# Kernel optimization log

Hardware: AMD Instinct MI355X
Metric: run time of the kernel (lower is better)

## Reference

```python
import jax, jax.numpy as jnp
import numpy as np

NEG_SLOPE = 0.2  # PyG GATConv default negative_slope


def gat_conv(x, src, dst, W, a_src, a_dst, bias, concat=True):
    """PyG-style GATConv (self-loops already appended to src/dst).
    x: [N, Fin], W: [Fin, H*C], a_src/a_dst: [H, C], bias: [H*C] or [C].
    """
    N = x.shape[0]
    H, C = a_src.shape
    h = (x @ W).reshape(N, H, C)                       # [N, H, C]
    s_src = jnp.einsum('nhc,hc->nh', h, a_src)         # per-node src logit
    s_dst = jnp.einsum('nhc,hc->nh', h, a_dst)         # per-node dst logit
    e = jax.nn.leaky_relu(s_src[src] + s_dst[dst], NEG_SLOPE)   # [E, H]
    # segment softmax over incoming edges of each destination node
    m = jax.ops.segment_max(e, dst, num_segments=N)    # [N, H]
    ex = jnp.exp(e - m[dst])
    denom = jax.ops.segment_sum(ex, dst, num_segments=N)
    alpha = ex / (denom[dst] + 1e-16)                  # [E, H]
    out = jax.ops.segment_sum(h[src] * alpha[:, :, None], dst, num_segments=N)  # [N,H,C]
    out = out.reshape(N, H * C) if concat else out.mean(axis=1)
    return out + bias


def setup_inputs() -> dict:
    key = jax.random.key(0)
    ks = jax.random.split(key, 12)
    N, E = 20000, 320000
    Fin, Hd, Hh = 384, 256, 4
    x = jax.random.normal(ks[0], (N, Fin), dtype=jnp.float32)
    edge_index = jax.random.randint(ks[1], (2, E), 0, N, dtype=jnp.int32)
    s = lambda k, shp, fan: jax.random.normal(k, shp, dtype=jnp.float32) / np.sqrt(fan)
    return {
        'x': x, 'edge_index': edge_index,
        'W1': s(ks[2], (Fin, Hh * Hd), Fin),
        'a_src1': s(ks[3], (Hh, Hd), Hd), 'a_dst1': s(ks[4], (Hh, Hd), Hd),
        'b1': jnp.zeros((Hh * Hd,), jnp.float32),
        'W2': s(ks[5], (Hh * Hd, Hd), Hh * Hd),
        'a_src2': s(ks[6], (1, Hd), Hd), 'a_dst2': s(ks[7], (1, Hd), Hd),
        'b2': jnp.zeros((Hd,), jnp.float32),
        'Wp1': s(ks[8], (Hd, Hd // 2), Hd), 'bp1': jnp.zeros((Hd // 2,), jnp.float32),
        'Wp2': s(ks[9], (Hd // 2, 1), Hd // 2), 'bp2': jnp.zeros((1,), jnp.float32),
    }


def reference(x, edge_index, W1, a_src1, a_dst1, b1, W2, a_src2, a_dst2, b2,
              Wp1, bp1, Wp2, bp2):
    N = x.shape[0]
    loops = jnp.arange(N, dtype=edge_index.dtype)
    src = jnp.concatenate([edge_index[0], loops])  # PyG add_self_loops=True
    dst = jnp.concatenate([edge_index[1], loops])
    h = jax.nn.elu(gat_conv(x, src, dst, W1, a_src1, a_dst1, b1, concat=True))
    h = jax.nn.elu(gat_conv(h, src, dst, W2, a_src2, a_dst2, b2, concat=True))
    graph_features = jnp.mean(h, axis=0, keepdims=True)  # batch=None path
    infl = jax.nn.sigmoid(jax.nn.relu(h @ Wp1 + bp1) @ Wp2 + bp2)
    return h, graph_features, infl
```

## Files before the change

kernel.cpp:

```cpp
#include <hip/hip_runtime.h>

#define NEG_SLOPE 0.2f

typedef __bf16 bf16x8 __attribute__((ext_vector_type(8)));
typedef float floatx4 __attribute__((ext_vector_type(4)));
typedef unsigned short ushortx4 __attribute__((ext_vector_type(4)));
typedef unsigned short ushortx8 __attribute__((ext_vector_type(8)));

__device__ __forceinline__ float eluf(float x) { return x > 0.f ? x : __expf(x) - 1.f; }
__device__ __forceinline__ float lrelu(float x) { return x > 0.f ? x : NEG_SLOPE * x; }

__device__ __forceinline__ unsigned short f2bf(float f) {
    unsigned u = __float_as_uint(f);
    u += 0x7FFFu + ((u >> 16) & 1u);
    return (unsigned short)(u >> 16);
}
__device__ __forceinline__ float bf2f(unsigned short h) {
    return __uint_as_float(((unsigned)h) << 16);
}

__device__ __forceinline__ void async16(const unsigned short* g, unsigned short* l) {
    __builtin_amdgcn_global_load_lds(
        (const __attribute__((address_space(1))) unsigned int*)g,
        (__attribute__((address_space(3))) unsigned int*)l,
        16, 0, 0);
}

__global__ __launch_bounds__(256) void prep_kernel(
        const int* __restrict__ ei, int E, int N, int* __restrict__ counts,
        const float* __restrict__ x, unsigned short* __restrict__ xb,
        const float* __restrict__ W1, unsigned short* __restrict__ w1t,
        const float* __restrict__ W2, unsigned short* __restrict__ w2t,
        const float* __restrict__ Wp1, unsigned short* __restrict__ wp1t,
        const float* __restrict__ as1, const float* __restrict__ ad1, float* __restrict__ U) {
    __shared__ float tile[32][33];
    int b = blockIdx.x;
    int t = threadIdx.x;
    int Et = E + N;
    int nA = (Et + 255) >> 8;
    int nB = (N * 96 + 255) >> 8;
    if (b < nA) {
        int i = b * 256 + t;
        if (i < Et) {
            int d = (i < E) ? ei[E + i] : (i - E);
            atomicAdd(&counts[d], 1);
        }
    } else if (b < nA + nB) {
        int i = (b - nA) * 256 + t;
        if (i < N * 96) {
            float4 v = ((const float4*)x)[i];
            ushortx4 o;
            o[0] = f2bf(v.x); o[1] = f2bf(v.y); o[2] = f2bf(v.z); o[3] = f2bf(v.w);
            *(ushortx4*)(xb + (size_t)i * 4) = o;
        }
    } else if (b < nA + nB + 384) {
        int idx = b - nA - nB;
        int n0 = (idx & 31) * 32, k0 = (idx >> 5) * 32;
        int tx = t & 31, ty = t >> 5;
        #pragma unroll
        for (int i = 0; i < 32; i += 8)
            tile[ty + i][tx] = W1[(size_t)(k0 + ty + i) * 1024 + n0 + tx];
        __syncthreads();
        #pragma unroll
        for (int i = 0; i < 32; i += 8)
            w1t[(size_t)(n0 + ty + i) * 384 + k0 + tx] = f2bf(tile[tx][ty + i]);
    } else if (b < nA + nB + 384 + 256) {
        int idx = b - nA - nB - 384;
        int n0 = (idx & 7) * 32, k0 = (idx >> 3) * 32;
        int tx = t & 31, ty = t >> 5;
        #pragma unroll
        for (int i = 0; i < 32; i += 8)
            tile[ty + i][tx] = W2[(size_t)(k0 + ty + i) * 256 + n0 + tx];
        __syncthreads();
        #pragma unroll
        for (int i = 0; i < 32; i += 8)
            w2t[(size_t)(n0 + ty + i) * 1024 + k0 + tx] = f2bf(tile[tx][ty + i]);
    } else if (b < nA + nB + 384 + 256 + 32) {
        int idx = b - nA - nB - 384 - 256;
        int n0 = (idx & 3) * 32, k0 = (idx >> 2) * 32;
        int tx = t & 31, ty = t >> 5;
        #pragma unroll
        for (int i = 0; i < 32; i += 8)
            tile[ty + i][tx] = Wp1[(size_t)(k0 + ty + i) * 128 + n0 + tx];
        __syncthreads();
        #pragma unroll
        for (int i = 0; i < 32; i += 8)
            wp1t[(size_t)(n0 + ty + i) * 256 + k0 + tx] = f2bf(tile[tx][ty + i]);
    } else {
        int idx = b - nA - nB - 384 - 256 - 32;
        int k = idx * 4 + (t >> 6);
        int lane = t & 63;
        #pragma unroll
        for (int r = 0; r < 8; r++) {
            int h = r & 3;
            const float* a = (r < 4 ? as1 : ad1) + h * 256 + lane * 4;
            const float* w = W1 + (size_t)k * 1024 + h * 256 + lane * 4;
            float4 wv = *(const float4*)w;
            float4 av = *(const float4*)a;
            float p = wv.x * av.x + wv.y * av.y + wv.z * av.z + wv.w * av.w;
            #pragma unroll
            for (int off = 32; off; off >>= 1) p += __shfl_xor(p, off);
            if (lane == 0) U[r * 384 + k] = p;
        }
    }
}

__global__ void scan_kernel(int* __restrict__ counts_cursor, int* __restrict__ row_ptr, int N) {
    __shared__ int s_wsum[16];
    __shared__ int s_carry;
    int t = threadIdx.x;
    int lane = t & 63, wid = t >> 6;
    if (t == 0) { s_carry = 0; row_ptr[0] = 0; }
    __syncthreads();
    for (int start = 0; start < N; start += 1024) {
        int i = start + t;
        int v = (i < N) ? counts_cursor[i] : 0;
        int s = v;
        #pragma unroll
        for (int d = 1; d < 64; d <<= 1) {
            int u = __shfl_up(s, d);
            if (lane >= d) s += u;
        }
        if (lane == 63) s_wsum[wid] = s;
        __syncthreads();
        if (wid == 0) {
            int w = (lane < 16) ? s_wsum[lane] : 0;
            #pragma unroll
            for (int d = 1; d < 16; d <<= 1) {
                int u = __shfl_up(w, d);
                if (lane >= d) w += u;
            }
            if (lane < 16) s_wsum[lane] = w;
        }
        __syncthreads();
        int incl = s + (wid ? s_wsum[wid - 1] : 0) + s_carry;
        if (i < N) { row_ptr[i + 1] = incl; counts_cursor[i] = incl - v; }
        __syncthreads();
        if (t == 0) s_carry += s_wsum[15];
        __syncthreads();
    }
}

__global__ void fill_kernel(const int* __restrict__ ei, int E, int N,
                            int* __restrict__ cursor, int* __restrict__ col) {
    int i = blockIdx.x * blockDim.x + threadIdx.x;
    int Et = E + N;
    if (i >= Et) return;
    int s, d;
    if (i < E) { s = ei[i]; d = ei[E + i]; } else { s = d = i - E; }
    int pos = atomicAdd(&cursor[d], 1);
    col[pos] = s;
}

__global__ void sU_kernel(const unsigned short* __restrict__ xb, const float* __restrict__ U,
                          float* __restrict__ ss1, float* __restrict__ sd1, int N) {
    int wid = (blockIdx.x * blockDim.x + threadIdx.x) >> 6;
    int lane = threadIdx.x & 63;
    if (wid >= N) return;
    int half = lane >> 5, l32 = lane & 31;
    int c0 = l32 * 12;
    const unsigned short* row = xb + (size_t)wid * 384 + c0;
    ushortx8 v8 = *(const ushortx8*)row;
    ushortx4 v4 = *(const ushortx4*)(row + 8);
    float xv[12];
    #pragma unroll
    for (int j = 0; j < 8; j++) xv[j] = bf2f(v8[j]);
    #pragma unroll
    for (int j = 0; j < 4; j++) xv[8 + j] = bf2f(v4[j]);
    float p[4];
    #pragma unroll
    for (int r = 0; r < 4; r++) {
        const float* u = U + (half * 4 + r) * 384 + c0;
        float s = 0.f;
        #pragma unroll
        for (int j = 0; j < 12; j++) s += xv[j] * u[j];
        #pragma unroll
        for (int off = 16; off; off >>= 1) s += __shfl_xor(s, off);
        p[r] = s;
    }
    if (l32 == 0) {
        float* dst = half ? (sd1 + wid * 4) : (ss1 + wid * 4);
        dst[0] = p[0]; dst[1] = p[1]; dst[2] = p[2]; dst[3] = p[3];
    }
}

__global__ void s2_kernel(const unsigned short* __restrict__ h2b, const float* __restrict__ a_src,
                          const float* __restrict__ a_dst, float* __restrict__ ssrc,
                          float* __restrict__ sdst, int N) {
    int wid = (blockIdx.x * blockDim.x + threadIdx.x) >> 6;
    int lane = threadIdx.x & 63;
    if (wid >= N) return;
    ushortx4 v = *(const ushortx4*)(h2b + (size_t)wid * 256 + lane * 4);
    float4 a = ((const float4*)a_src)[lane];
    float4 d = ((const float4*)a_dst)[lane];
    float v0 = bf2f(v[0]), v1 = bf2f(v[1]), v2 = bf2f(v[2]), v3 = bf2f(v[3]);
    float s = v0 * a.x + v1 * a.y + v2 * a.z + v3 * a.w;
    float t = v0 * d.x + v1 * d.y + v2 * d.z + v3 * d.w;
    for (int off = 32; off; off >>= 1) { s += __shfl_xor(s, off); t += __shfl_xor(t, off); }
    if (lane == 0) { ssrc[wid] = s; sdst[wid] = t; }
}

__global__ __launch_bounds__(256) void alpha1_kernel(const float* __restrict__ ssrc,
        const float* __restrict__ sdst, const int* __restrict__ row_ptr,
        const int* __restrict__ col, float* __restrict__ wx, float* __restrict__ den, int N) {
    int wid = (blockIdx.x * blockDim.x + threadIdx.x) >> 6;
    int lane = threadIdx.x & 63;
    if (wid >= N) return;
    int base = row_ptr[wid];
    int deg = row_ptr[wid + 1] - base;
    float sd0 = sdst[wid * 4 + 0], sd1 = sdst[wid * 4 + 1];
    float sd2 = sdst[wid * 4 + 2], sd3 = sdst[wid * 4 + 3];
    float m0 = -1e30f, m1 = -1e30f, m2 = -1e30f, m3 = -1e30f;
    for (int i = lane; i < deg; i += 64) {
        int s = col[base + i];
        const float* sp = ssrc + s * 4;
        m0 = fmaxf(m0, lrelu(sp[0] + sd0));
        m1 = fmaxf(m1, lrelu(sp[1] + sd1));
        m2 = fmaxf(m2, lrelu(sp[2] + sd2));
        m3 = fmaxf(m3, lrelu(sp[3] + sd3));
    }
    #pragma unroll
    for (int off = 32; off; off >>= 1) {
        m0 = fmaxf(m0, __shfl_xor(m0, off));
        m1 = fmaxf(m1, __shfl_xor(m1, off));
        m2 = fmaxf(m2, __shfl_xor(m2, off));
        m3 = fmaxf(m3, __shfl_xor(m3, off));
    }
    float d0 = 0.f, d1 = 0.f, d2 = 0.f, d3 = 0.f;
    for (int i = lane; i < deg; i += 64) {
        int s = col[base + i];
        const float* sp = ssrc + s * 4;
        float4 w4;
        w4.x = __expf(lrelu(sp[0] + sd0) - m0); d0 += w4.x;
        w4.y = __expf(lrelu(sp[1] + sd1) - m1); d1 += w4.y;
        w4.z = __expf(lrelu(sp[2] + sd2) - m2); d2 += w4.z;
        w4.w = __expf(lrelu(sp[3] + sd3) - m3); d3 += w4.w;
        *(float4*)(wx + (size_t)(base + i) * 4) = w4;
    }
    #pragma unroll
    for (int off = 32; off; off >>= 1) {
        d0 += __shfl_xor(d0, off);
        d1 += __shfl_xor(d1, off);
        d2 += __shfl_xor(d2, off);
        d3 += __shfl_xor(d3, off);
    }
    if (lane == 0) {
        den[wid * 4 + 0] = d0; den[wid * 4 + 1] = d1;
        den[wid * 4 + 2] = d2; den[wid * 4 + 3] = d3;
    }
}

__global__ __launch_bounds__(256) void alpha2_kernel(const float* __restrict__ ssrc,
        const float* __restrict__ sdst, const int* __restrict__ row_ptr,
        const int* __restrict__ col, float* __restrict__ wx, float* __restrict__ den, int N) {
    int wid = (blockIdx.x * blockDim.x + threadIdx.x) >> 6;
    int lane = threadIdx.x & 63;
    if (wid >= N) return;
    int base = row_ptr[wid];
    int deg = row_ptr[wid + 1] - base;
    float sd = sdst[wid];
    float m = -1e30f;
    for (int i = lane; i < deg; i += 64) {
        int s = col[base + i];
        m = fmaxf(m, lrelu(ssrc[s] + sd));
    }
    #pragma unroll
    for (int off = 32; off; off >>= 1) m = fmaxf(m, __shfl_xor(m, off));
    float d = 0.f;
    for (int i = lane; i < deg; i += 64) {
        int s = col[base + i];
        float x = __expf(lrelu(ssrc[s] + sd) - m);
        d += x;
        wx[base + i] = x;
    }
    #pragma unroll
    for (int off = 32; off; off >>= 1) d += __shfl_xor(d, off);
    if (lane == 0) den[wid] = d;
}

__global__ __launch_bounds__(256) void aggx_kernel(const unsigned short* __restrict__ xb,
        const float* __restrict__ wx, const float* __restrict__ den,
        const int* __restrict__ row_ptr, const int* __restrict__ col,
        unsigned short* __restrict__ aggxn, int N) {
    __shared__ unsigned short lds[4][1536];
    int t = threadIdx.x;
    int wv = t >> 6;
    int wid = blockIdx.x * 4 + wv;
    int lane = t & 63;
    bool active = wid < N;
    int half = lane >> 5, l32 = lane & 31;
    int c0 = l32 * 12;
    if (active) {
        int base = row_ptr[wid];
        int deg = row_ptr[wid + 1] - base;
        float acc[4][12] = {};
        for (int i = half; i < deg; i += 2) {
            int e = base + i;
            int s = col[e];
            float4 w4 = *(const float4*)(wx + (size_t)e * 4);
            const unsigned short* row = xb + (size_t)s * 384 + c0;
            ushortx8 v8 = *(const ushortx8*)row;
            ushortx4 v4 = *(const ushortx4*)(row + 8);
            float xv[12];
            #pragma unroll
            for (int j = 0; j < 8; j++) xv[j] = bf2f(v8[j]);
            #pragma unroll
            for (int j = 0; j < 4; j++) xv[8 + j] = bf2f(v4[j]);
            #pragma unroll
            for (int j = 0; j < 12; j++) {
                acc[0][j] += w4.x * xv[j];
                acc[1][j] += w4.y * xv[j];
                acc[2][j] += w4.z * xv[j];
                acc[3][j] += w4.w * xv[j];
            }
        }
        #pragma unroll
        for (int h = 0; h < 4; h++)
            #pragma unroll
            for (int j = 0; j < 12; j++)
                acc[h][j] += __shfl_xor(acc[h][j], 32);
        #pragma unroll
        for (int hh = 0; hh < 2; hh++) {
            int h = half * 2 + hh;
            float inv = 1.f / (den[wid * 4 + h] + 1e-16f);
            ushortx8 o8; ushortx4 o4;
            #pragma unroll
            for (int j = 0; j < 8; j++) {
                float v = half ? acc[2 + hh][j] : acc[hh][j];
                o8[j] = f2bf(v * inv);
            }
            #pragma unroll
            for (int j = 0; j < 4; j++) {
                float v = half ? acc[2 + hh][8 + j] : acc[hh][8 + j];
                o4[j] = f2bf(v * inv);
            }
            unsigned short* lp = &lds[wv][h * 384 + c0];
            *(ushortx8*)lp = o8;
            *(ushortx4*)(lp + 8) = o4;
        }
    }
    __syncthreads();
    size_t blockBase = (size_t)blockIdx.x * 4 * 1536;
    const unsigned short* lflat = &lds[0][0];
    #pragma unroll
    for (int j = 0; j < 3; j++) {
        int so = j * 2048 + t * 8;
        int node = blockIdx.x * 4 + so / 1536;
        if (node < N)
            *(ushortx8*)(aggxn + blockBase + so) = *(const ushortx8*)(lflat + so);
    }
}

#define LDK 40

__global__ __launch_bounds__(256) void gemm_l1(const unsigned short* __restrict__ A,
        const unsigned short* __restrict__ Bt, const float* __restrict__ bias,
        unsigned short* __restrict__ Cout, int M) {
    __shared__ unsigned short As[2][128 * 32];
    __shared__ unsigned short Bs[2][128 * 32];
    int t = threadIdx.x;
    int lane = t & 63, wave = t >> 6;
    int wm = (wave >> 1) * 64, wn = (wave & 1) * 64;
    int q = lane >> 4, l16 = lane & 15;
    int row0 = blockIdx.y * 128, col0 = blockIdx.x * 128;
    int hoff = (col0 >> 8) * 384;
    floatx4 acc[4][4] = {};
    int srow = t >> 2, skc = (t & 3) * 8;
    const unsigned short* Ag0 = A + (size_t)min(row0 + srow, M - 1) * 1536 + hoff + skc;
    const unsigned short* Ag1 = A + (size_t)min(row0 + srow + 64, M - 1) * 1536 + hoff + skc;
    const unsigned short* Bg0 = Bt + (size_t)(col0 + srow) * 384 + skc;
    const unsigned short* Bg1 = Bt + (size_t)(col0 + srow + 64) * 384 + skc;
#define STG_L1(buf, kt) \
    async16(Ag0 + (kt), &As[buf][t * 8]); \
    async16(Ag1 + (kt), &As[buf][2048 + t * 8]); \
    async16(Bg0 + (kt), &Bs[buf][t * 8]); \
    async16(Bg1 + (kt), &Bs[buf][2048 + t * 8]);
    STG_L1(0, 0)
    __syncthreads();
    #pragma unroll
    for (int ti = 0; ti < 12; ++ti) {
        int cur = ti & 1;
        if (ti < 11) { STG_L1(cur ^ 1, (ti + 1) * 32) }
        __builtin_amdgcn_sched_barrier(0);
        bf16x8 af[4], bfr[4];
        #pragma unroll
        for (int i = 0; i < 4; i++)
            af[i] = *(const bf16x8*)&As[cur][(wm + i * 16 + l16) * 32 + q * 8];
        #pragma unroll
        for (int j = 0; j < 4; j++)
            bfr[j] = *(const bf16x8*)&Bs[cur][(wn + j * 16 + l16) * 32 + q * 8];
        #pragma unroll
        for (int i = 0; i < 4; i++)
            #pragma unroll
            for (int j = 0; j < 4; j++)
                acc[i][j] = __builtin_amdgcn_mfma_f32_16x16x32_bf16(af[i], bfr[j], acc[i][j], 0, 0, 0);
        __syncthreads();
    }
#undef STG_L1
    float bj[4];
    #pragma unroll
    for (int j = 0; j < 4; j++) bj[j] = bias[col0 + wn + l16 + j * 16];
    #pragma unroll
    for (int i = 0; i < 4; i++) {
        #pragma unroll
        for (int r = 0; r < 4; r++) {
            int grow = row0 + wm + i * 16 + q * 4 + r;
            if (grow < M) {
                unsigned short* cp = Cout + (size_t)grow * 1024 + col0 + wn + l16;
                #pragma unroll
                for (int j = 0; j < 4; j++) cp[j * 16] = f2bf(eluf(acc[i][j][r] + bj[j]));
            }
        }
    }
}

__global__ __launch_bounds__(256) void gemm_l2(const unsigned short* __restrict__ A,
        const unsigned short* __restrict__ Bt, unsigned short* __restrict__ Cout, int M) {
    __shared__ unsigned short As[2][128 * 32];
    __shared__ unsigned short Bs[2][64 * 32];
    int t = threadIdx.x;
    int lane = t & 63, wave = t >> 6;
    int wm = (wave >> 1) * 64, wn = (wave & 1) * 32;
    int q = lane >> 4, l16 = lane & 15;
    int row0 = blockIdx.y * 128, col0 = blockIdx.x * 64;
    floatx4 acc[4][2] = {};
    int srow = t >> 2, skc = (t & 3) * 8;
    const unsigned short* Ag0 = A + (size_t)min(row0 + srow, M - 1) * 1024 + skc;
    const unsigned short* Ag1 = A + (size_t)min(row0 + srow + 64, M - 1) * 1024 + skc;
    const unsigned short* Bg0 = Bt + (size_t)(col0 + srow) * 1024 + skc;
#define STG_L2(buf, kt) \
    async16(Ag0 + (kt), &As[buf][t * 8]); \
    async16(Ag1 + (kt), &As[buf][2048 + t * 8]); \
    async16(Bg0 + (kt), &Bs[buf][t * 8]);
    STG_L2(0, 0)
    __syncthreads();
    #pragma unroll
    for (int ti = 0; ti < 32; ++ti) {
        int cur = ti & 1;
        if (ti < 31) { STG_L2(cur ^ 1, (ti + 1) * 32) }
        __builtin_amdgcn_sched_barrier(0);
        bf16x8 af[4], bfr[2];
        #pragma unroll
        for (int i = 0; i < 4; i++)
            af[i] = *(const bf16x8*)&As[cur][(wm + i * 16 + l16) * 32 + q * 8];
        #pragma unroll
        for (int j = 0; j < 2; j++)
            bfr[j] = *(const bf16x8*)&Bs[cur][(wn + j * 16 + l16) * 32 + q * 8];
        #pragma unroll
        for (int i = 0; i < 4; i++)
            #pragma unroll
            for (int j = 0; j < 2; j++)
                acc[i][j] = __builtin_amdgcn_mfma_f32_16x16x32_bf16(af[i], bfr[j], acc[i][j], 0, 0, 0);
        __syncthreads();
    }
#undef STG_L2
    #pragma unroll
    for (int i = 0; i < 4; i++) {
        #pragma unroll
        for (int r = 0; r < 4; r++) {
            int grow = row0 + wm + i * 16 + q * 4 + r;
            if (grow < M) {
                unsigned short* cp = Cout + (size_t)grow * 256 + col0 + wn + l16;
                #pragma unroll
                for (int j = 0; j < 2; j++) cp[j * 16] = f2bf(acc[i][j][r]);
            }
        }
    }
}

__global__ __launch_bounds__(256) void agg2_kernel(const unsigned short* __restrict__ h2b,
        const float* __restrict__ wx, const float* __restrict__ den,
        const int* __restrict__ row_ptr, const int* __restrict__ col,
        const float* __restrict__ bias, float* __restrict__ out,
        unsigned short* __restrict__ outb, int N) {
    int wid = (blockIdx.x * blockDim.x + threadIdx.x) >> 6;
    int lane = threadIdx.x & 63;
    if (wid >= N) return;
    int base = row_ptr[wid];
    int deg = row_ptr[wid + 1] - base;
    float4 a = {0, 0, 0, 0};
    int c = lane * 4;
    int i = 0;
    for (; i + 1 < deg; i += 2) {
        int s0 = col[base + i], s1 = col[base + i + 1];
        float x0 = wx[base + i], x1 = wx[base + i + 1];
        ushortx4 v0 = *(const ushortx4*)(h2b + (size_t)s0 * 256 + c);
        ushortx4 v1 = *(const ushortx4*)(h2b + (size_t)s1 * 256 + c);
        a.x += x0 * bf2f(v0[0]) + x1 * bf2f(v1[0]);
        a.y += x0 * bf2f(v0[1]) + x1 * bf2f(v1[1]);
        a.z += x0 * bf2f(v0[2]) + x1 * bf2f(v1[2]);
        a.w += x0 * bf2f(v0[3]) + x1 * bf2f(v1[3]);
    }
    if (i < deg) {
        int s0 = col[base + i];
        float x0 = wx[base + i];
        ushortx4 v0 = *(const ushortx4*)(h2b + (size_t)s0 * 256 + c);
        a.x += x0 * bf2f(v0[0]); a.y += x0 * bf2f(v0[1]);
        a.z += x0 * bf2f(v0[2]); a.w += x0 * bf2f(v0[3]);
    }
    float inv = 1.f / (den[wid] + 1e-16f);
    float4 o;
    o.x = eluf(a.x * inv + bias[c + 0]);
    o.y = eluf(a.y * inv + bias[c + 1]);
    o.z = eluf(a.z * inv + bias[c + 2]);
    o.w = eluf(a.w * inv + bias[c + 3]);
    *(float4*)(out + (size_t)wid * 256 + c) = o;
    ushortx4 ob;
    ob[0] = f2bf(o.x); ob[1] = f2bf(o.y); ob[2] = f2bf(o.z); ob[3] = f2bf(o.w);
    *(ushortx4*)(outb + (size_t)wid * 256 + c) = ob;
}

__global__ __launch_bounds__(256) void tail_kernel(const float* __restrict__ h,
        const unsigned short* __restrict__ hbf, const unsigned short* __restrict__ wp1t,
        const float* __restrict__ bp1, const float* __restrict__ Wp2,
        const float* __restrict__ bp2, float* __restrict__ gf, float* __restrict__ infl, int M) {
    int b = blockIdx.x;
    int nInfl = (M + 127) / 128;
    if (b < nInfl) {
        __shared__ unsigned short As[128 * LDK];
        __shared__ unsigned short Bs[128 * LDK];
        __shared__ float partial[2][128];
        int t = threadIdx.x;
        int lane = t & 63, wave = t >> 6;
        int wm = (wave >> 1) * 64, wn = (wave & 1) * 64;
        int q = lane >> 4, l16 = lane & 15;
        int row0 = b * 128;
        floatx4 acc[4][4] = {};
        int sg = (t & 7) * 4;
        int sr = t >> 3;
        for (int kt = 0; kt < 256; kt += 32) {
            #pragma unroll
            for (int p = 0; p < 4; p++) {
                int r = sr + p * 32;
                int ga = min(row0 + r, M - 1);
                *(ushortx4*)&As[r * LDK + sg] = *(const ushortx4*)(hbf + (size_t)ga * 256 + kt + sg);
                *(ushortx4*)&Bs[r * LDK + sg] = *(const ushortx4*)(wp1t + (size_t)r * 256 + kt + sg);
            }
            __syncthreads();
            bf16x8 af[4], bfr[4];
            #pragma unroll
            for (int i = 0; i < 4; i++)
                af[i] = *(const bf16x8*)&As[(wm + i * 16 + l16) * LDK + q * 8];
            #pragma unroll
            for (int j = 0; j < 4; j++)
                bfr[j] = *(const bf16x8*)&Bs[(wn + j * 16 + l16) * LDK + q * 8];
            #pragma unroll
            for (int i = 0; i < 4; i++)
                #pragma unroll
                for (int j = 0; j < 4; j++)
                    acc[i][j] = __builtin_amdgcn_mfma_f32_16x16x32_bf16(af[i], bfr[j], acc[i][j], 0, 0, 0);
            __syncthreads();
        }
        float b1v[4], w2v[4];
        #pragma unroll
        for (int j = 0; j < 4; j++) {
            int colj = wn + j * 16 + l16;
            b1v[j] = bp1[colj];
            w2v[j] = Wp2[colj];
        }
        #pragma unroll
        for (int i = 0; i < 4; i++) {
            #pragma unroll
            for (int r = 0; r < 4; r++) {
                float s = fmaxf(acc[i][0][r] + b1v[0], 0.f) * w2v[0]
                        + fmaxf(acc[i][1][r] + b1v[1], 0.f) * w2v[1]
                        + fmaxf(acc[i][2][r] + b1v[2], 0.f) * w2v[2]
                        + fmaxf(acc[i][3][r] + b1v[3], 0.f) * w2v[3];
                #pragma unroll
                for (int off = 1; off < 16; off <<= 1) s += __shfl_xor(s, off);
                if (l16 == 0) partial[wave & 1][wm + i * 16 + q * 4 + r] = s;
            }
        }
        __syncthreads();
        if (t < 128) {
            int row = row0 + t;
            if (row < M) {
                float v = partial[0][t] + partial[1][t] + bp2[0];
                infl[row] = 1.f / (1.f + __expf(-v));
            }
        }
    } else {
        int bb = b - nInfl;
        int c = threadIdx.x;
        int per = (M + 159) / 160;
        int n0 = bb * per;
        int n1 = min(M, n0 + per);
        float a0 = 0.f, a1 = 0.f, a2 = 0.f, a3 = 0.f;
        float a4 = 0.f, a5 = 0.f, a6 = 0.f, a7 = 0.f;
        int n = n0;
        for (; n + 8 <= n1; n += 8) {
            a0 += h[(size_t)(n + 0) * 256 + c];
            a1 += h[(size_t)(n + 1) * 256 + c];
            a2 += h[(size_t)(n + 2) * 256 + c];
            a3 += h[(size_t)(n + 3) * 256 + c];
            a4 += h[(size_t)(n + 4) * 256 + c];
            a5 += h[(size_t)(n + 5) * 256 + c];
            a6 += h[(size_t)(n + 6) * 256 + c];
            a7 += h[(size_t)(n + 7) * 256 + c];
        }
        for (; n < n1; n++) a0 += h[(size_t)n * 256 + c];
        float acc = ((a0 + a1) + (a2 + a3)) + ((a4 + a5) + (a6 + a7));
        atomicAdd(&gf[c], acc * (1.0f / M));
    }
}

extern "C" void kernel_launch(void* const* d_in, const int* in_sizes, int n_in,
                              void* d_out, int out_size, void* d_ws, size_t ws_size,
                              hipStream_t stream) {
    const float* x   = (const float*)d_in[0];
    const int*   ei  = (const int*)d_in[1];
    const float* W1  = (const float*)d_in[2];
    const float* as1 = (const float*)d_in[3];
    const float* ad1 = (const float*)d_in[4];
    const float* b1  = (const float*)d_in[5];
    const float* W2  = (const float*)d_in[6];
    const float* as2 = (const float*)d_in[7];
    const float* ad2 = (const float*)d_in[8];
    const float* b2  = (const float*)d_in[9];
    const float* Wp1 = (const float*)d_in[10];
    const float* bp1 = (const float*)d_in[11];
    const float* Wp2 = (const float*)d_in[12];
    const float* bp2 = (const float*)d_in[13];

    const int N  = in_sizes[0] / 384;
    const int E  = in_sizes[1] / 2;
    const int Et = E + N;

    char* wsp = (char*)d_ws;
    unsigned short* xb    = (unsigned short*)wsp; wsp += (size_t)N * 384  * sizeof(short);
    unsigned short* aggxn = (unsigned short*)wsp; wsp += (size_t)N * 1536 * sizeof(short);
    unsigned short* h1eb  = (unsigned short*)wsp; wsp += (size_t)N * 1024 * sizeof(short);
    unsigned short* h2b   = (unsigned short*)wsp; wsp += (size_t)N * 256  * sizeof(short);
    unsigned short* hbf   = (unsigned short*)wsp; wsp += (size_t)N * 256  * sizeof(short);
    unsigned short* w1t   = (unsigned short*)wsp; wsp += (size_t)1024 * 384 * sizeof(short);
    unsigned short* w2t   = (unsigned short*)wsp; wsp += (size_t)256 * 1024 * sizeof(short);
    unsigned short* wp1t  = (unsigned short*)wsp; wsp += (size_t)128 * 256 * sizeof(short);
    float* U   = (float*)wsp; wsp += (size_t)8 * 384 * sizeof(float);
    float* ss1 = (float*)wsp; wsp += (size_t)N * 4 * sizeof(float);
    float* sd1 = (float*)wsp; wsp += (size_t)N * 4 * sizeof(float);
    float* ss2 = (float*)wsp; wsp += (size_t)N * sizeof(float);
    float* sd2 = (float*)wsp; wsp += (size_t)N * sizeof(float);
    float* den1 = (float*)wsp; wsp += (size_t)N * 4 * sizeof(float);
    float* den2 = (float*)wsp; wsp += (size_t)N * sizeof(float);
    float* wx1  = (float*)wsp; wsp += (size_t)Et * 4 * sizeof(float);
    float* wx2  = (float*)wsp; wsp += (size_t)Et * sizeof(float);
    int* row_ptr = (int*)wsp; wsp += (size_t)(N + 1) * sizeof(int);
    int* cursor  = (int*)wsp; wsp += (size_t)N * sizeof(int);
    int* col     = (int*)wsp;

    float* out_h  = (float*)d_out;
    float* out_gf = out_h + (size_t)N * 256;
    float* out_if = out_gf + 256;

    hipMemsetAsync(cursor, 0, (size_t)N * sizeof(int), stream);
    int nA = (Et + 255) / 256;
    int nB = (N * 96 + 255) / 256;
    int nPrep = nA + nB + 384 + 256 + 32 + 96;
    prep_kernel<<<nPrep, 256, 0, stream>>>(ei, E, N, cursor, x, xb, W1, w1t, W2, w2t, Wp1, wp1t, as1, ad1, U);
    scan_kernel<<<1, 1024, 0, stream>>>(cursor, row_ptr, N);
    fill_kernel<<<nA, 256, 0, stream>>>(ei, E, N, cursor, col);

    sU_kernel<<<(N + 3) / 4, 256, 0, stream>>>(xb, U, ss1, sd1, N);
    alpha1_kernel<<<(N + 3) / 4, 256, 0, stream>>>(ss1, sd1, row_ptr, col, wx1, den1, N);
    aggx_kernel<<<(N + 3) / 4, 256, 0, stream>>>(xb, wx1, den1, row_ptr, col, aggxn, N);
    gemm_l1<<<dim3(8, (N + 127) / 128), 256, 0, stream>>>(aggxn, w1t, b1, h1eb, N);

    gemm_l2<<<dim3(4, (N + 127) / 128), 256, 0, stream>>>(h1eb, w2t, h2b, N);
    s2_kernel<<<(N + 3) / 4, 256, 0, stream>>>(h2b, as2, ad2, ss2, sd2, N);
    alpha2_kernel<<<(N + 3) / 4, 256, 0, stream>>>(ss2, sd2, row_ptr, col, wx2, den2, N);
    agg2_kernel<<<(N + 3) / 4, 256, 0, stream>>>(h2b, wx2, den2, row_ptr, col, b2, out_h, hbf, N);

    hipMemsetAsync(out_gf, 0, 256 * sizeof(float), stream);
    tail_kernel<<<(N + 127) / 128 + 160, 256, 0, stream>>>(out_h, hbf, wp1t, bp1, Wp2, bp2, out_gf, out_if, N);
}
```

Before: 357.8 us.

## Fuse edge softmax into aggregation kernels and prefetch neighbor rows via shuffles

Removes the separate alpha1 and alpha2 kernels. Each aggregation wave now computes the per-destination max, the exponentials and the denominator itself. Edge weights and source indices are broadcast across lanes with shuffles, and the next neighbor row is software-prefetched before the current one is accumulated. This eliminates two launches and the global write and read of the per-edge weight arrays, at the cost of extra shuffle work and an extra ss pass inside the aggregation kernels.

Measured after the change: 351.7 us. No clear change (-1.7%).

```diff
diff --git a/kernel.cpp b/kernel.cpp
--- a/kernel.cpp
+++ b/kernel.cpp
@@ -200,86 +200,8 @@
     if (lane == 0) { ssrc[wid] = s; sdst[wid] = t; }
 }
 
-__global__ __launch_bounds__(256) void alpha1_kernel(const float* __restrict__ ssrc,
-        const float* __restrict__ sdst, const int* __restrict__ row_ptr,
-        const int* __restrict__ col, float* __restrict__ wx, float* __restrict__ den, int N) {
-    int wid = (blockIdx.x * blockDim.x + threadIdx.x) >> 6;
-    int lane = threadIdx.x & 63;
-    if (wid >= N) return;
-    int base = row_ptr[wid];
-    int deg = row_ptr[wid + 1] - base;
-    float sd0 = sdst[wid * 4 + 0], sd1 = sdst[wid * 4 + 1];
-    float sd2 = sdst[wid * 4 + 2], sd3 = sdst[wid * 4 + 3];
-    float m0 = -1e30f, m1 = -1e30f, m2 = -1e30f, m3 = -1e30f;
-    for (int i = lane; i < deg; i += 64) {
-        int s = col[base + i];
-        const float* sp = ssrc + s * 4;
-        m0 = fmaxf(m0, lrelu(sp[0] + sd0));
-        m1 = fmaxf(m1, lrelu(sp[1] + sd1));
-        m2 = fmaxf(m2, lrelu(sp[2] + sd2));
-        m3 = fmaxf(m3, lrelu(sp[3] + sd3));
-    }
-    #pragma unroll
-    for (int off = 32; off; off >>= 1) {
-        m0 = fmaxf(m0, __shfl_xor(m0, off));
-        m1 = fmaxf(m1, __shfl_xor(m1, off));
-        m2 = fmaxf(m2, __shfl_xor(m2, off));
-        m3 = fmaxf(m3, __shfl_xor(m3, off));
-    }
-    float d0 = 0.f, d1 = 0.f, d2 = 0.f, d3 = 0.f;
-    for (int i = lane; i < deg; i += 64) {
-        int s = col[base + i];
-        const float* sp = ssrc + s * 4;
-        float4 w4;
-        w4.x = __expf(lrelu(sp[0] + sd0) - m0); d0 += w4.x;
-        w4.y = __expf(lrelu(sp[1] + sd1) - m1); d1 += w4.y;
-        w4.z = __expf(lrelu(sp[2] + sd2) - m2); d2 += w4.z;
-        w4.w = __expf(lrelu(sp[3] + sd3) - m3); d3 += w4.w;
-        *(float4*)(wx + (size_t)(base + i) * 4) = w4;
-    }
-    #pragma unroll
-    for (int off = 32; off; off >>= 1) {
-        d0 += __shfl_xor(d0, off);
-        d1 += __shfl_xor(d1, off);
-        d2 += __shfl_xor(d2, off);
-        d3 += __shfl_xor(d3, off);
-    }
-    if (lane == 0) {
-        den[wid * 4 + 0] = d0; den[wid * 4 + 1] = d1;
-        den[wid * 4 + 2] = d2; den[wid * 4 + 3] = d3;
-    }
-}
-
-__global__ __launch_bounds__(256) void alpha2_kernel(const float* __restrict__ ssrc,
-        const float* __restrict__ sdst, const int* __restrict__ row_ptr,
-        const int* __restrict__ col, float* __restrict__ wx, float* __restrict__ den, int N) {
-    int wid = (blockIdx.x * blockDim.x + threadIdx.x) >> 6;
-    int lane = threadIdx.x & 63;
-    if (wid >= N) return;
-    int base = row_ptr[wid];
-    int deg = row_ptr[wid + 1] - base;
-    float sd = sdst[wid];
-    float m = -1e30f;
-    for (int i = lane; i < deg; i += 64) {
-        int s = col[base + i];
-        m = fmaxf(m, lrelu(ssrc[s] + sd));
-    }
-    #pragma unroll
-    for (int off = 32; off; off >>= 1) m = fmaxf(m, __shfl_xor(m, off));
-    float d = 0.f;
-    for (int i = lane; i < deg; i += 64) {
-        int s = col[base + i];
-        float x = __expf(lrelu(ssrc[s] + sd) - m);
-        d += x;
-        wx[base + i] = x;
-    }
-    #pragma unroll
-    for (int off = 32; off; off >>= 1) d += __shfl_xor(d, off);
-    if (lane == 0) den[wid] = d;
-}
-
 __global__ __launch_bounds__(256) void aggx_kernel(const unsigned short* __restrict__ xb,
-        const float* __restrict__ wx, const float* __restrict__ den,
+        const float* __restrict__ ss1, const float* __restrict__ sd1,
         const int* __restrict__ row_ptr, const int* __restrict__ col,
         unsigned short* __restrict__ aggxn, int N) {
     __shared__ unsigned short lds[4][1536];
@@ -290,39 +212,99 @@
     bool active = wid < N;
     int half = lane >> 5, l32 = lane & 31;
     int c0 = l32 * 12;
+    float4 dsum = {0.f, 0.f, 0.f, 0.f};
+    float acc[4][12] = {};
     if (active) {
         int base = row_ptr[wid];
         int deg = row_ptr[wid + 1] - base;
-        float acc[4][12] = {};
-        for (int i = half; i < deg; i += 2) {
-            int e = base + i;
-            int s = col[e];
-            float4 w4 = *(const float4*)(wx + (size_t)e * 4);
-            const unsigned short* row = xb + (size_t)s * 384 + c0;
-            ushortx8 v8 = *(const ushortx8*)row;
-            ushortx4 v4 = *(const ushortx4*)(row + 8);
-            float xv[12];
-            #pragma unroll
-            for (int j = 0; j < 8; j++) xv[j] = bf2f(v8[j]);
-            #pragma unroll
-            for (int j = 0; j < 4; j++) xv[8 + j] = bf2f(v4[j]);
-            #pragma unroll
-            for (int j = 0; j < 12; j++) {
-                acc[0][j] += w4.x * xv[j];
-                acc[1][j] += w4.y * xv[j];
-                acc[2][j] += w4.z * xv[j];
-                acc[3][j] += w4.w * xv[j];
-            }
+        float4 sd = *(const float4*)(sd1 + (size_t)wid * 4);
+        float4 mx = {-1e30f, -1e30f, -1e30f, -1e30f};
+        for (int chunk = 0; chunk < deg; chunk += 64) {
+            int cl = chunk + lane;
+            if (cl < deg) {
+                int s = col[base + cl];
+                float4 sp = *(const float4*)(ss1 + (size_t)s * 4);
+                mx.x = fmaxf(mx.x, lrelu(sp.x + sd.x));
+                mx.y = fmaxf(mx.y, lrelu(sp.y + sd.y));
+                mx.z = fmaxf(mx.z, lrelu(sp.z + sd.z));
+                mx.w = fmaxf(mx.w, lrelu(sp.w + sd.w));
+            }
+        }
+        #pragma unroll
+        for (int off = 32; off; off >>= 1) {
+            mx.x = fmaxf(mx.x, __shfl_xor(mx.x, off));
+            mx.y = fmaxf(mx.y, __shfl_xor(mx.y, off));
+            mx.z = fmaxf(mx.z, __shfl_xor(mx.z, off));
+            mx.w = fmaxf(mx.w, __shfl_xor(mx.w, off));
+        }
+        for (int chunk = 0; chunk < deg; chunk += 64) {
+            int cnt = min(64, deg - chunk);
+            int cl = chunk + lane;
+            int myS = 0;
+            float4 myW = {0.f, 0.f, 0.f, 0.f};
+            if (cl < deg) {
+                myS = col[base + cl];
+                float4 sp = *(const float4*)(ss1 + (size_t)myS * 4);
+                myW.x = __expf(lrelu(sp.x + sd.x) - mx.x); dsum.x += myW.x;
+                myW.y = __expf(lrelu(sp.y + sd.y) - mx.y); dsum.y += myW.y;
+                myW.z = __expf(lrelu(sp.z + sd.z) - mx.z); dsum.z += myW.z;
+                myW.w = __expf(lrelu(sp.w + sd.w) - mx.w); dsum.w += myW.w;
+            }
+            int K = (cnt + 1) >> 1;
+            int jj = half;
+            int js = min(jj, cnt - 1);
+            int s = __shfl(myS, js);
+            float4 nw;
+            nw.x = __shfl(myW.x, js); nw.y = __shfl(myW.y, js);
+            nw.z = __shfl(myW.z, js); nw.w = __shfl(myW.w, js);
+            if (jj >= cnt) { nw.x = 0.f; nw.y = 0.f; nw.z = 0.f; nw.w = 0.f; }
+            const unsigned short* r = xb + (size_t)s * 384 + c0;
+            ushortx8 n8 = *(const ushortx8*)r;
+            ushortx4 n4 = *(const ushortx4*)(r + 8);
+            for (int k = 0; k < K; k++) {
+                ushortx8 c8 = n8; ushortx4 cc = n4; float4 cw = nw;
+                jj = (k + 1) * 2 + half;
+                js = min(jj, cnt - 1);
+                s = __shfl(myS, js);
+                nw.x = __shfl(myW.x, js); nw.y = __shfl(myW.y, js);
+                nw.z = __shfl(myW.z, js); nw.w = __shfl(myW.w, js);
+                if (jj >= cnt) { nw.x = 0.f; nw.y = 0.f; nw.z = 0.f; nw.w = 0.f; }
+                r = xb + (size_t)s * 384 + c0;
+                n8 = *(const ushortx8*)r;
+                n4 = *(const ushortx4*)(r + 8);
+                float xv[12];
+                #pragma unroll
+                for (int j = 0; j < 8; j++) xv[j] = bf2f(c8[j]);
+                #pragma unroll
+                for (int j = 0; j < 4; j++) xv[8 + j] = bf2f(cc[j]);
+                #pragma unroll
+                for (int j = 0; j < 12; j++) {
+                    acc[0][j] += cw.x * xv[j];
+                    acc[1][j] += cw.y * xv[j];
+                    acc[2][j] += cw.z * xv[j];
+                    acc[3][j] += cw.w * xv[j];
+                }
+            }
+        }
+        #pragma unroll
+        for (int off = 32; off; off >>= 1) {
+            dsum.x += __shfl_xor(dsum.x, off);
+            dsum.y += __shfl_xor(dsum.y, off);
+            dsum.z += __shfl_xor(dsum.z, off);
+            dsum.w += __shfl_xor(dsum.w, off);
         }
         #pragma unroll
         for (int h = 0; h < 4; h++)
             #pragma unroll
             for (int j = 0; j < 12; j++)
                 acc[h][j] += __shfl_xor(acc[h][j], 32);
+        float dsel0 = half ? dsum.z : dsum.x;
+        float dsel1 = half ? dsum.w : dsum.y;
         #pragma unroll
         for (int hh = 0; hh < 2; hh++) {
             int h = half * 2 + hh;
-            float inv = 1.f / (den[wid * 4 + h] + 1e-16f);
+            float dh = hh ? dsel1 : dsel0;
+            float inv = 1.f / (dh + 1e-16f);
             ushortx8 o8; ushortx4 o4;
             #pragma unroll
             for (int j = 0; j < 8; j++) {
@@ -469,7 +451,7 @@
 }
 
 __global__ __launch_bounds__(256) void agg2_kernel(const unsigned short* __restrict__ h2b,
-        const float* __restrict__ wx, const float* __restrict__ den,
+        const float* __restrict__ ss2, const float* __restrict__ sd2,
         const int* __restrict__ row_ptr, const int* __restrict__ col,
         const float* __restrict__ bias, float* __restrict__ out,
         unsigned short* __restrict__ outb, int N) {
@@ -478,36 +460,68 @@
     if (wid >= N) return;
     int base = row_ptr[wid];
     int deg = row_ptr[wid + 1] - base;
-    float4 a = {0, 0, 0, 0};
-    int c = lane * 4;
-    int i = 0;
-    for (; i + 1 < deg; i += 2) {
-        int s0 = col[base + i], s1 = col[base + i + 1];
-        float x0 = wx[base + i], x1 = wx[base + i + 1];
-        ushortx4 v0 = *(const ushortx4*)(h2b + (size_t)s0 * 256 + c);
-        ushortx4 v1 = *(const ushortx4*)(h2b + (size_t)s1 * 256 + c);
-        a.x += x0 * bf2f(v0[0]) + x1 * bf2f(v1[0]);
-        a.y += x0 * bf2f(v0[1]) + x1 * bf2f(v1[1]);
-        a.z += x0 * bf2f(v0[2]) + x1 * bf2f(v1[2]);
-        a.w += x0 * bf2f(v0[3]) + x1 * bf2f(v1[3]);
-    }
-    if (i < deg) {
-        int s0 = col[base + i];
-        float x0 = wx[base + i];
-        ushortx4 v0 = *(const ushortx4*)(h2b + (size_t)s0 * 256 + c);
-        a.x += x0 * bf2f(v0[0]); a.y += x0 * bf2f(v0[1]);
-        a.z += x0 * bf2f(v0[2]); a.w += x0 * bf2f(v0[3]);
-    }
-    float inv = 1.f / (den[wid] + 1e-16f);
+    float sd = sd2[wid];
+    float m = -1e30f;
+    for (int chunk = 0; chunk < deg; chunk += 64) {
+        int cl = chunk + lane;
+        if (cl < deg) {
+            int s = col[base + cl];
+            m = fmaxf(m, lrelu(ss2[s] + sd));
+        }
+    }
+    #pragma unroll
+    for (int off = 32; off; off >>= 1) m = fmaxf(m, __shfl_xor(m, off));
+    float4 a = {0.f, 0.f, 0.f, 0.f};
+    float dsum = 0.f;
+    int ch = lane * 4;
+    for (int chunk = 0; chunk < deg; chunk += 64) {
+        int cnt = min(64, deg - chunk);
+        int cl = chunk + lane;
+        int myS = 0;
+        float myW = 0.f;
+        if (cl < deg) {
+            myS = col[base + cl];
+            myW = __expf(lrelu(ss2[myS] + sd) - m);
+            dsum += myW;
+        }
+        int K = (cnt + 1) >> 1;
+        int j1 = min(1, cnt - 1);
+        int s0 = __shfl(myS, 0);
+        int s1 = __shfl(myS, j1);
+        float w0 = __shfl(myW, 0);
+        float w1 = __shfl(myW, j1);
+        if (cnt < 2) w1 = 0.f;
+        ushortx4 n0 = *(const ushortx4*)(h2b + (size_t)s0 * 256 + ch);
+        ushortx4 n1 = *(const ushortx4*)(h2b + (size_t)s1 * 256 + ch);
+        for (int k = 0; k < K; k++) {
+            ushortx4 v0 = n0, v1 = n1;
+            float cw0 = w0, cw1 = w1;
+            int e0 = (k + 1) * 2, e1 = e0 + 1;
+            int js0 = min(e0, cnt - 1), js1 = min(e1, cnt - 1);
+            int t0 = __shfl(myS, js0), t1 = __shfl(myS, js1);
+            w0 = __shfl(myW, js0); w1 = __shfl(myW, js1);
+            if (e0 >= cnt) w0 = 0.f;
+            if (e1 >= cnt) w1 = 0.f;
+            n0 = *(const ushortx4*)(h2b + (size_t)t0 * 256 + ch);
+            n1 = *(const ushortx4*)(h2b + (size_t)t1 * 256 + ch);
+            a.x += cw0 * bf2f(v0[0]) + cw1 * bf2f(v1[0]);
+            a.y += cw0 * bf2f(v0[1]) + cw1 * bf2f(v1[1]);
+            a.z += cw0 * bf2f(v0[2]) + cw1 * bf2f(v1[2]);
+            a.w += cw0 * bf2f(v0[3]) + cw1 * bf2f(v1[3]);
+        }
+    }
+    #pragma unroll
+    for (int off = 32; off; off >>= 1) dsum += __shfl_xor(dsum, off);
+    float inv = 1.f / (dsum + 1e-16f);
     float4 o;
-    o.x = eluf(a.x * inv + bias[c + 0]);
-    o.y = eluf(a.y * inv + bias[c + 1]);
-    o.z = eluf(a.z * inv + bias[c + 2]);
-    o.w = eluf(a.w * inv + bias[c + 3]);
-    *(float4*)(out + (size_t)wid * 256 + c) = o;
+    o.x = eluf(a.x * inv + bias[ch + 0]);
+    o.y = eluf(a.y * inv + bias[ch + 1]);
+    o.z = eluf(a.z * inv + bias[ch + 2]);
+    o.w = eluf(a.w * inv + bias[ch + 3]);
+    *(float4*)(out + (size_t)wid * 256 + ch) = o;
     ushortx4 ob;
     ob[0] = f2bf(o.x); ob[1] = f2bf(o.y); ob[2] = f2bf(o.z); ob[3] = f2bf(o.w);
-    *(ushortx4*)(outb + (size_t)wid * 256 + c) = ob;
+    *(ushortx4*)(outb + (size_t)wid * 256 + ch) = ob;
 }
 
 __global__ __launch_bounds__(256) void tail_kernel(const float* __restrict__ h,
@@ -640,10 +654,6 @@
     float* sd1 = (float*)wsp; wsp += (size_t)N * 4 * sizeof(float);
     float* ss2 = (float*)wsp; wsp += (size_t)N * sizeof(float);
     float* sd2 = (float*)wsp; wsp += (size_t)N * sizeof(float);
-    float* den1 = (float*)wsp; wsp += (size_t)N * 4 * sizeof(float);
-    float* den2 = (float*)wsp; wsp += (size_t)N * sizeof(float);
-    float* wx1  = (float*)wsp; wsp += (size_t)Et * 4 * sizeof(float);
-    float* wx2  = (float*)wsp; wsp += (size_t)Et * sizeof(float);
     int* row_ptr = (int*)wsp; wsp += (size_t)(N + 1) * sizeof(int);
     int* cursor  = (int*)wsp; wsp += (size_t)N * sizeof(int);
     int* col     = (int*)wsp;
@@ -661,14 +671,12 @@
     fill_kernel<<<nA, 256, 0, stream>>>(ei, E, N, cursor, col);
 
     sU_kernel<<<(N + 3) / 4, 256, 0, stream>>>(xb, U, ss1, sd1, N);
-    alpha1_kernel<<<(N + 3) / 4, 256, 0, stream>>>(ss1, sd1, row_ptr, col, wx1, den1, N);
-    aggx_kernel<<<(N + 3) / 4, 256, 0, stream>>>(xb, wx1, den1, row_ptr, col, aggxn, N);
+    aggx_kernel<<<(N + 3) / 4, 256, 0, stream>>>(xb, ss1, sd1, row_ptr, col, aggxn, N);
     gemm_l1<<<dim3(8, (N + 127) / 128), 256, 0, stream>>>(aggxn, w1t, b1, h1eb, N);
 
     gemm_l2<<<dim3(4, (N + 127) / 128), 256, 0, stream>>>(h1eb, w2t, h2b, N);
     s2_kernel<<<(N + 3) / 4, 256, 0, stream>>>(h2b, as2, ad2, ss2, sd2, N);
-    alpha2_kernel<<<(N + 3) / 4, 256, 0, stream>>>(ss2, sd2, row_ptr, col, wx2, den2, N);
-    agg2_kernel<<<(N + 3) / 4, 256, 0, stream>>>(h2b, wx2, den2, row_ptr, col, b2, out_h, hbf, N);
+    agg2_kernel<<<(N + 3) / 4, 256, 0, stream>>>(h2b, ss2, sd2, row_ptr, col, b2, out_h, hbf, N);
 
     hipMemsetAsync(out_gf, 0, 256 * sizeof(float), stream);
     tail_kernel<<<(N + 127) / 128 + 160, 256, 0, stream>>>(out_h, hbf, wp1t, bp1, Wp2, bp2, out_gf, out_if, N);
```
